# Performance work log

Measured on AMD Instinct MI355X. Metric: run time of the kernel, lower is better.

The kernel has to match this reference:

```python
import jax, jax.numpy as jnp
import numpy as np

N = 10000      # nodes
E = 160000     # edges
F_IN = 128     # input_feature
G = 64         # graphs in batch
NC = 10        # num_classes
H1, H2, H3 = 1000, 700, 200


def _xavier(k, fi, fo):
    lim = float(np.sqrt(6.0 / (fi + fo)))
    return jax.random.uniform(k, (fi, fo), jnp.float32, -lim, lim)


def setup_inputs() -> dict:
    key = jax.random.key(0)
    ks = jax.random.split(key, 8)
    x = jax.random.normal(ks[0], (N, F_IN), jnp.float32)
    edge_index = jax.random.randint(ks[1], (2, E), 0, N)
    batch = jnp.sort(jax.random.randint(ks[2], (N,), 0, G))
    return {
        "x": x,
        "edge_index": edge_index,
        "batch": batch,
        "W1": _xavier(ks[3], F_IN, H1), "b1": jnp.zeros((H1,), jnp.float32),
        "W2": _xavier(ks[4], H1, H2),   "b2": jnp.zeros((H2,), jnp.float32),
        "W3": _xavier(ks[5], H2, H3),   "b3": jnp.zeros((H3,), jnp.float32),
        "Wl": _xavier(ks[6], H3, NC),   "bl": jnp.zeros((NC,), jnp.float32),
    }


def _gcn_conv(x, W, b, src, dst, dinv):
    # GCNConv: h = xW; out_i = sum_{j->i} d_j^-1/2 d_i^-1/2 h_j + d_i^-1 h_i + b
    h = x @ W
    coef = dinv[src] * dinv[dst]                      # [E]
    agg = jax.ops.segment_sum(h[src] * coef[:, None], dst, num_segments=N)
    agg = agg + h * (dinv * dinv)[:, None]            # self-loop term
    return agg + b


def reference(x, edge_index, batch, W1, b1, W2, b2, W3, b3, Wl, bl):
    src, dst = edge_index[0], edge_index[1]
    # degree with self-loops (edge weight 1), computed on target nodes
    deg = jax.ops.segment_sum(jnp.ones((E,), x.dtype), dst, num_segments=N) + 1.0
    dinv = jax.lax.rsqrt(deg)

    h = jax.nn.relu(_gcn_conv(x, W1, b1, src, dst, dinv))
    h = jax.nn.relu(_gcn_conv(h, W2, b2, src, dst, dinv))
    h = jax.nn.relu(_gcn_conv(h, W3, b3, src, dst, dinv))

    # global_mean_pool over graph ids
    s = jax.ops.segment_sum(h, batch, num_segments=G)
    cnt = jax.ops.segment_sum(jnp.ones((N,), h.dtype), batch, num_segments=G)
    pooled = s / jnp.maximum(cnt, 1.0)[:, None]

    # dropout is identity in eval mode
    return pooled @ Wl + bl
```

## Files before the change

kernel.cpp:

```cpp
#include <hip/hip_runtime.h>
#include <hip/hip_bf16.h>
#include <stdint.h>


#define SLOT 64

__device__ __forceinline__ uint16_t f2b(float f) {
    union { float f; uint32_t u; } v; v.f = f;
    return (uint16_t)((v.u + 0x7fffu + ((v.u >> 16) & 1u)) >> 16);
}
__device__ __forceinline__ float blo(uint32_t u) { union { uint32_t u; float f; } v; v.u = u << 16; return v.f; }
__device__ __forceinline__ float bhi(uint32_t u) { union { uint32_t u; float f; } v; v.u = u & 0xffff0000u; return v.f; }

__global__ void k_scatter(const int* __restrict__ src, const int* __restrict__ dst,
                          int* __restrict__ cursor, int* __restrict__ slots, int E) {
    int e = blockIdx.x * blockDim.x + threadIdx.x;
    if (e < E) {
        int s = src[e], d = dst[e];
        int pos = atomicAdd(&cursor[d], 1);
        if (pos < SLOT) slots[d * SLOT + pos] = s;
    }
}

__global__ void k_prep(const float* __restrict__ W1, const float* __restrict__ W2,
                       const float* __restrict__ W3,
                       uint16_t* __restrict__ T1, uint16_t* __restrict__ T2,
                       uint16_t* __restrict__ T3,
                       const float* __restrict__ b1, const float* __restrict__ b2,
                       const float* __restrict__ b3,
                       float* __restrict__ p1, float* __restrict__ p2,
                       float* __restrict__ p3,
                       const float* __restrict__ x, uint16_t* __restrict__ xb,
                       const int* __restrict__ deg, float* __restrict__ dinv,
                       int N, int F, int H1, int H2, int H3,
                       int Fp, int H1p, int H2p, int H3p, int n8) {
    __shared__ float tile[32][33];
    int z = blockIdx.z;
    if (z < 3) {
        const float* W; uint16_t* T; int K, Nn, Kp, Np;
        if (z == 0)      { W = W1; T = T1; K = F;  Nn = H1; Kp = Fp;  Np = H1p; }
        else if (z == 1) { W = W2; T = T2; K = H1; Nn = H2; Kp = H1p; Np = H2p; }
        else             { W = W3; T = T3; K = H2; Nn = H3; Kp = H2p; Np = H3p; }
        if ((int)blockIdx.x * 32 >= Kp || (int)blockIdx.y * 32 >= Np) return;
        int k0 = blockIdx.x * 32, n0 = blockIdx.y * 32;
        int tx = threadIdx.x, ty = threadIdx.y;
        for (int i = ty; i < 32; i += 8) {
            int k = k0 + i, n = n0 + tx;
            tile[i][tx] = (k < K && n < Nn) ? W[(size_t)k * Nn + n] : 0.f;
        }
        __syncthreads();
        for (int i = ty; i < 32; i += 8) {
            int n = n0 + i, k = k0 + tx;
            T[(size_t)n * Kp + k] = f2b(tile[tx][i]);
        }
    } else {
        int id = (blockIdx.y * gridDim.x + blockIdx.x) * 256 + threadIdx.y * 32 + threadIdx.x;
        if (z == 3) {
            if (id < H1p) p1[id] = (id < H1) ? b1[id] : 0.f;
            else if (id < H1p + H2p) { int k = id - H1p; p2[k] = (k < H2) ? b2[k] : 0.f; }
            else if (id < H1p + H2p + H3p) { int k = id - H1p - H2p; p3[k] = (k < H3) ? b3[k] : 0.f; }
        } else if (z == 4) {
            if (id < n8) {
                int node = id / (F >> 3);
                float dv = rsqrtf((float)deg[node] + 1.0f);
                const float4* x4 = (const float4*)x;
                float4 a = x4[2 * id], b = x4[2 * id + 1];
                uint4 o;
                o.x = (uint32_t)f2b(a.x * dv) | ((uint32_t)f2b(a.y * dv) << 16);
                o.y = (uint32_t)f2b(a.z * dv) | ((uint32_t)f2b(a.w * dv) << 16);
                o.z = (uint32_t)f2b(b.x * dv) | ((uint32_t)f2b(b.y * dv) << 16);
                o.w = (uint32_t)f2b(b.z * dv) | ((uint32_t)f2b(b.w * dv) << 16);
                ((uint4*)xb)[id] = o;
            }
        } else {
            if (id < N) dinv[id] = rsqrtf((float)deg[id] + 1.0f);
        }
    }
}

__global__ __launch_bounds__(256) void k_agg_panel(
    const uint16_t* __restrict__ in, uint16_t* __restrict__ out,
    const int* __restrict__ deg_, const int* __restrict__ slots,
    const float* __restrict__ dinv, const float* __restrict__ bias,
    int N, int Hc, int pc, int P, int relu) {
    int slotg = blockIdx.x & 7;
    int panel = slotg % P;
    int seg   = slotg / P;
    int nseg  = 8 / P;
    int segLen = (N + nseg - 1) / nseg;
    int wave = threadIdx.x >> 6, lane = threadIdx.x & 63;
    int half = lane >> 5, sub = lane & 31;
    int item = (blockIdx.x >> 3) * 128 + wave * 32 + sub;
    int rel = item / pc;
    if (rel >= segLen) return;
    int node = seg * segLen + rel;
    if (node >= N) return;
    int j = panel * pc + (item - rel * pc);
    int deg = deg_[node];
    if (deg > SLOT) deg = SLOT;
    int base = node * SLOT;
    float dv = dinv[node];
    const uint4* in4 = (const uint4*)in;
    float a[8] = {0.f, 0.f, 0.f, 0.f, 0.f, 0.f, 0.f, 0.f};
    if (half == 0) {
        uint4 v = in4[(size_t)node * Hc + j];
        a[0] = blo(v.x); a[1] = bhi(v.x);
        a[2] = blo(v.y); a[3] = bhi(v.y);
        a[4] = blo(v.z); a[5] = bhi(v.z);
        a[6] = blo(v.w); a[7] = bhi(v.w);
    }
    int D8 = deg & ~7;
    int e = 4 * half;
    if (e < D8) {
        int4 q = *(const int4*)&slots[base + e];
        uint4 h0 = in4[(size_t)q.x * Hc + j];
        uint4 h1 = in4[(size_t)q.y * Hc + j];
        uint4 h2 = in4[(size_t)q.z * Hc + j];
        uint4 h3 = in4[(size_t)q.w * Hc + j];
        for (e += 8; e < D8; e += 8) {
            int4 qn = *(const int4*)&slots[base + e];
            uint4 g0 = in4[(size_t)qn.x * Hc + j];
            uint4 g1 = in4[(size_t)qn.y * Hc + j];
            uint4 g2 = in4[(size_t)qn.z * Hc + j];
            uint4 g3 = in4[(size_t)qn.w * Hc + j];
            a[0] += blo(h0.x); a[1] += bhi(h0.x);
            a[2] += blo(h0.y); a[3] += bhi(h0.y);
            a[4] += blo(h0.z); a[5] += bhi(h0.z);
            a[6] += blo(h0.w); a[7] += bhi(h0.w);
            a[0] += blo(h1.x); a[1] += bhi(h1.x);
            a[2] += blo(h1.y); a[3] += bhi(h1.y);
            a[4] += blo(h1.z); a[5] += bhi(h1.z);
            a[6] += blo(h1.w); a[7] += bhi(h1.w);
            a[0] += blo(h2.x); a[1] += bhi(h2.x);
            a[2] += blo(h2.y); a[3] += bhi(h2.y);
            a[4] += blo(h2.z); a[5] += bhi(h2.z);
            a[6] += blo(h2.w); a[7] += bhi(h2.w);
            a[0] += blo(h3.x); a[1] += bhi(h3.x);
            a[2] += blo(h3.y); a[3] += bhi(h3.y);
            a[4] += blo(h3.z); a[5] += bhi(h3.z);
            a[6] += blo(h3.w); a[7] += bhi(h3.w);
            h0 = g0; h1 = g1; h2 = g2; h3 = g3;
        }
        a[0] += blo(h0.x); a[1] += bhi(h0.x);
        a[2] += blo(h0.y); a[3] += bhi(h0.y);
        a[4] += blo(h0.z); a[5] += bhi(h0.z);
        a[6] += blo(h0.w); a[7] += bhi(h0.w);
        a[0] += blo(h1.x); a[1] += bhi(h1.x);
        a[2] += blo(h1.y); a[3] += bhi(h1.y);
        a[4] += blo(h1.z); a[5] += bhi(h1.z);
        a[6] += blo(h1.w); a[7] += bhi(h1.w);
        a[0] += blo(h2.x); a[1] += bhi(h2.x);
        a[2] += blo(h2.y); a[3] += bhi(h2.y);
        a[4] += blo(h2.z); a[5] += bhi(h2.z);
        a[6] += blo(h2.w); a[7] += bhi(h2.w);
        a[0] += blo(h3.x); a[1] += bhi(h3.x);
        a[2] += blo(h3.y); a[3] += bhi(h3.y);
        a[4] += blo(h3.z); a[5] += bhi(h3.z);
        a[6] += blo(h3.w); a[7] += bhi(h3.w);
    }
    int t0 = half ? (D8 + 4 < deg ? D8 + 4 : deg) : D8;
    int t1 = half ? deg : (D8 + 4 < deg ? D8 + 4 : deg);
    for (int ee = t0; ee < t1; ++ee) {
        int s0 = slots[base + ee];
        uint4 h = in4[(size_t)s0 * Hc + j];
        a[0] += blo(h.x); a[1] += bhi(h.x);
        a[2] += blo(h.y); a[3] += bhi(h.y);
        a[4] += blo(h.z); a[5] += bhi(h.z);
        a[6] += blo(h.w); a[7] += bhi(h.w);
    }
#pragma unroll
    for (int t = 0; t < 8; ++t) a[t] += __shfl_xor(a[t], 32, 64);
    if (half == 0) {
        if (bias) {
            const float4* b4 = (const float4*)bias;
            float4 b0 = b4[2 * j], b1 = b4[2 * j + 1];
            a[0] = fmaf(a[0], dv, b0.x); a[1] = fmaf(a[1], dv, b0.y);
            a[2] = fmaf(a[2], dv, b0.z); a[3] = fmaf(a[3], dv, b0.w);
            a[4] = fmaf(a[4], dv, b1.x); a[5] = fmaf(a[5], dv, b1.y);
            a[6] = fmaf(a[6], dv, b1.z); a[7] = fmaf(a[7], dv, b1.w);
        } else {
#pragma unroll
            for (int t = 0; t < 8; ++t) a[t] *= dv;
        }
        if (relu) {
#pragma unroll
            for (int t = 0; t < 8; ++t) a[t] = fmaxf(a[t], 0.f);
        }
        uint4 o;
        o.x = (uint32_t)f2b(a[0]) | ((uint32_t)f2b(a[1]) << 16);
        o.y = (uint32_t)f2b(a[2]) | ((uint32_t)f2b(a[3]) << 16);
        o.z = (uint32_t)f2b(a[4]) | ((uint32_t)f2b(a[5]) << 16);
        o.w = (uint32_t)f2b(a[6]) | ((uint32_t)f2b(a[7]) << 16);
        ((uint4*)out)[(size_t)node * Hc + j] = o;
    }
}

__global__ __launch_bounds__(256) void k_pool_fast(
    const uint16_t* __restrict__ h, const int* __restrict__ batch,
    float* __restrict__ pooled_sum, int N, int H, int Hp) {
    int j    = threadIdx.x & 63;
    int slot = threadIdx.x >> 6;
    int Hc   = H >> 2;
    if (j >= Hc) return;
    int HcP  = Hp >> 2;
    const uint2* h2 = (const uint2*)h;
    int base = (blockIdx.x * 4 + slot) * 16;
    float a0 = 0.f, a1 = 0.f, a2 = 0.f, a3 = 0.f;
    int gcur = -1;
#pragma unroll 4
    for (int t = 0; t < 16; ++t) {
        int node = base + t;
        if (node < N) {
            int g = batch[node];
            if (g != gcur) {
                if (gcur >= 0) {
                    float* ps = &pooled_sum[(size_t)gcur * H + j * 4];
                    atomicAdd(&ps[0], a0); atomicAdd(&ps[1], a1);
                    atomicAdd(&ps[2], a2); atomicAdd(&ps[3], a3);
                }
                gcur = g; a0 = a1 = a2 = a3 = 0.f;
            }
            uint2 v = h2[(size_t)node * HcP + j];
            a0 += blo(v.x); a1 += bhi(v.x);
            a2 += blo(v.y); a3 += bhi(v.y);
        }
    }
    if (gcur >= 0) {
        float* ps = &pooled_sum[(size_t)gcur * H + j * 4];
        atomicAdd(&ps[0], a0); atomicAdd(&ps[1], a1);
        atomicAdd(&ps[2], a2); atomicAdd(&ps[3], a3);
    }
}

typedef __attribute__((ext_vector_type(8))) short short8;
typedef __attribute__((ext_vector_type(4))) float floatx4;

#define LDSP(p) ((__attribute__((address_space(3))) void*)(uintptr_t)(p))
#define GLBP(p) ((const __attribute__((address_space(1))) void*)(uintptr_t)(p))

__global__ __launch_bounds__(256) void k_gemm128(
    const uint16_t* __restrict__ A, const uint16_t* __restrict__ Bt,
    const float* __restrict__ bias, uint16_t* __restrict__ Cout,
    int M, int Kp, int Np, int relu, int nrg, int nr,
    const float* __restrict__ rowscale) {
    int bid = blockIdx.x;
    int rsub = bid & 7;
    int t_ = bid >> 3;
    int rg = t_ % nrg, cc = t_ / nrg;
    int rt = rg * 8 + rsub;
    if (rt >= nr) return;
    int row0 = rt * 128, col0 = cc * 128;

    __shared__ uint16_t As[128 * 64];
    __shared__ uint16_t Bs[128 * 64];
    int tid = threadIdx.x;
    int wave = tid >> 6, lane = tid & 63;
    int quad = lane >> 4, m16 = lane & 15;
    int wr = wave >> 1, wc = wave & 1;

    int rA = tid >> 3;
    int cA = (tid & 7) ^ (rA & 7);
    const uint16_t* gA = A  + (size_t)(row0 + rA) * Kp + cA * 8;
    const uint16_t* gB = Bt + (size_t)(col0 + rA) * Kp + cA * 8;
    uint16_t* lA = As + tid * 8;
    uint16_t* lB = Bs + tid * 8;
    size_t rowStep32 = (size_t)32 * Kp;

    floatx4 acc[4][4];
#pragma unroll
    for (int i = 0; i < 4; ++i)
#pragma unroll
        for (int j = 0; j < 4; ++j) acc[i][j] = (floatx4){0.f, 0.f, 0.f, 0.f};

    const short* Ash = (const short*)As;
    const short* Bsh = (const short*)Bs;
    int swA = m16 & 7;

    for (int k0 = 0; k0 < Kp; k0 += 64) {
#pragma unroll
        for (int p = 0; p < 4; ++p) {
            __builtin_amdgcn_global_load_lds(GLBP(gA + p * rowStep32), LDSP(lA + p * 2048), 16, 0, 0);
            __builtin_amdgcn_global_load_lds(GLBP(gB + p * rowStep32), LDSP(lB + p * 2048), 16, 0, 0);
        }
        gA += 64; gB += 64;
        __syncthreads();
#pragma unroll
        for (int h = 0; h < 2; ++h) {
            short8 af[4], bf[4];
            int c = h * 4 + quad;
            int pos = (c ^ swA) * 8;
#pragma unroll
            for (int i = 0; i < 4; ++i)
                af[i] = *(const short8*)&Ash[(wr * 64 + i * 16 + m16) * 64 + pos];
#pragma unroll
            for (int j = 0; j < 4; ++j)
                bf[j] = *(const short8*)&Bsh[(wc * 64 + j * 16 + m16) * 64 + pos];
#pragma unroll
            for (int i = 0; i < 4; ++i)
#pragma unroll
                for (int j = 0; j < 4; ++j)
                    acc[i][j] = __builtin_amdgcn_mfma_f32_16x16x32_bf16(af[i], bf[j], acc[i][j], 0, 0, 0);
        }
        __syncthreads();
    }

    float bv[4];
#pragma unroll
    for (int j = 0; j < 4; ++j) {
        int n = col0 + wc * 64 + j * 16 + m16;
        bv[j] = bias ? bias[n] : 0.f;
    }
#pragma unroll
    for (int i = 0; i < 4; ++i) {
        int mBase = row0 + wr * 64 + i * 16 + quad * 4;
#pragma unroll
        for (int r = 0; r < 4; ++r) {
            int m = mBase + r;
            if (m < M) {
                float s = rowscale ? rowscale[m] : 1.f;
#pragma unroll
                for (int j = 0; j < 4; ++j) {
                    int n = col0 + wc * 64 + j * 16 + m16;
                    float v = acc[i][j][r] * s + bv[j];
                    if (relu) v = fmaxf(v, 0.f);
                    Cout[(size_t)m * Np + n] = f2b(v);
                }
            }
        }
    }
}

__global__ __launch_bounds__(256) void k_gemm64(
    const uint16_t* __restrict__ A, const uint16_t* __restrict__ Bt,
    const float* __restrict__ bias, uint16_t* __restrict__ Cout,
    int M, int Kp, int Np, int relu, int nrg, int nr,
    const float* __restrict__ rowscale) {
    int bid = blockIdx.x;
    int rsub = bid & 7;
    int t_ = bid >> 3;
    int rg = t_ % nrg, cc = t_ / nrg;
    int rt = rg * 8 + rsub;
    if (rt >= nr) return;
    int row0 = rt * 128, col0 = cc * 64;

    __shared__ uint16_t As[128 * 64];
    __shared__ uint16_t Bs[64 * 64];
    int tid = threadIdx.x;
    int wave = tid >> 6, lane = tid & 63;
    int quad = lane >> 4, m16 = lane & 15;
    int wr = wave >> 1, wc = wave & 1;

    int rA = tid >> 3;
    int cA = (tid & 7) ^ (rA & 7);
    const uint16_t* gA = A  + (size_t)(row0 + rA) * Kp + cA * 8;
    const uint16_t* gB = Bt + (size_t)(col0 + rA) * Kp + cA * 8;
    uint16_t* lA = As + tid * 8;
    uint16_t* lB = Bs + tid * 8;
    size_t rowStep32 = (size_t)32 * Kp;

    floatx4 acc[4][2];
#pragma unroll
    for (int i = 0; i < 4; ++i)
#pragma unroll
        for (int j = 0; j < 2; ++j) acc[i][j] = (floatx4){0.f, 0.f, 0.f, 0.f};

    const short* Ash = (const short*)As;
    const short* Bsh = (const short*)Bs;
    int swA = m16 & 7;

    for (int k0 = 0; k0 < Kp; k0 += 64) {
#pragma unroll
        for (int p = 0; p < 4; ++p)
            __builtin_amdgcn_global_load_lds(GLBP(gA + p * rowStep32), LDSP(lA + p * 2048), 16, 0, 0);
#pragma unroll
        for (int p = 0; p < 2; ++p)
            __builtin_amdgcn_global_load_lds(GLBP(gB + p * rowStep32), LDSP(lB + p * 2048), 16, 0, 0);
        gA += 64; gB += 64;
        __syncthreads();
#pragma unroll
        for (int h = 0; h < 2; ++h) {
            short8 af[4], bf[2];
            int c = h * 4 + quad;
            int pos = (c ^ swA) * 8;
#pragma unroll
            for (int i = 0; i < 4; ++i)
                af[i] = *(const short8*)&Ash[(wr * 64 + i * 16 + m16) * 64 + pos];
#pragma unroll
            for (int j = 0; j < 2; ++j)
                bf[j] = *(const short8*)&Bsh[(wc * 32 + j * 16 + m16) * 64 + pos];
#pragma unroll
            for (int i = 0; i < 4; ++i)
#pragma unroll
                for (int j = 0; j < 2; ++j)
                    acc[i][j] = __builtin_amdgcn_mfma_f32_16x16x32_bf16(af[i], bf[j], acc[i][j], 0, 0, 0);
        }
        __syncthreads();
    }

    float bv[2];
#pragma unroll
    for (int j = 0; j < 2; ++j) {
        int n = col0 + wc * 32 + j * 16 + m16;
        bv[j] = bias ? bias[n] : 0.f;
    }
#pragma unroll
    for (int i = 0; i < 4; ++i) {
        int mBase = row0 + wr * 64 + i * 16 + quad * 4;
#pragma unroll
        for (int r = 0; r < 4; ++r) {
            int m = mBase + r;
            if (m < M) {
                float s = rowscale ? rowscale[m] : 1.f;
#pragma unroll
                for (int j = 0; j < 2; ++j) {
                    int n = col0 + wc * 32 + j * 16 + m16;
                    float v = acc[i][j][r] * s + bv[j];
                    if (relu) v = fmaxf(v, 0.f);
                    Cout[(size_t)m * Np + n] = f2b(v);
                }
            }
        }
    }
}

__global__ void k_classifier(const float* __restrict__ pooled_sum,
                             const int* __restrict__ batch,
                             const float* __restrict__ Wl, const float* __restrict__ bl,
                             float* __restrict__ out, int N, int H, int NC) {
    int g = blockIdx.x, c = threadIdx.x;
    int lo = 0, hi = N;
    while (lo < hi) { int mid = (lo + hi) >> 1; if (batch[mid] < g) lo = mid + 1; else hi = mid; }
    int start = lo;
    lo = start; hi = N;
    while (lo < hi) { int mid = (lo + hi) >> 1; if (batch[mid] < g + 1) lo = mid + 1; else hi = mid; }
    int end = lo;
    float scale = 1.0f / fmaxf((float)(end - start), 1.0f);
    if (c < NC) {
        float acc = 0.f;
        for (int k = 0; k < H; ++k) acc += pooled_sum[(size_t)g * H + k] * Wl[(size_t)k * NC + c];
        out[(size_t)g * NC + c] = acc * scale + bl[c];
    }
}

static inline size_t align256(size_t x) { return (x + 255) & ~(size_t)255; }
static inline int pad128(int x) { return (x + 127) & ~127; }

extern "C" void kernel_launch(void* const* d_in, const int* in_sizes, int n_in,
                              void* d_out, int out_size, void* d_ws, size_t ws_size,
                              hipStream_t stream) {
    const float* x   = (const float*)d_in[0];
    const int*   ei  = (const int*)d_in[1];
    const int*   bat = (const int*)d_in[2];
    const float* W1  = (const float*)d_in[3];
    const float* b1  = (const float*)d_in[4];
    const float* W2  = (const float*)d_in[5];
    const float* b2  = (const float*)d_in[6];
    const float* W3  = (const float*)d_in[7];
    const float* b3  = (const float*)d_in[8];
    const float* Wl  = (const float*)d_in[9];
    const float* bl  = (const float*)d_in[10];

    const int N  = in_sizes[2];
    const int E  = in_sizes[1] / 2;
    const int F  = in_sizes[0] / N;
    const int H1 = in_sizes[4];
    const int H2 = in_sizes[6];
    const int H3 = in_sizes[8];
    const int NC = in_sizes[10];
    const int G  = out_size / NC;
    const int* src = ei;
    const int* dst = ei + E;

    const int Mp  = pad128(N);
    const int Fp  = F;
    const int H1p = pad128(H1);
    const int H2p = pad128(H2);
    const int H3p = pad128(H3);

    char* p = (char*)d_ws;
    size_t off = 0;
    auto carve = [&](size_t bytes) { void* q = p + off; off += align256(bytes); return q; };
    uint16_t* xb     = (uint16_t*)carve((size_t)Mp * Fp * 2);
    uint16_t* bufA   = (uint16_t*)carve((size_t)Mp * 2048);
    uint16_t* bufB   = (uint16_t*)carve((size_t)Mp * 2048);
    uint16_t* W1t    = (uint16_t*)carve((size_t)H1p * Fp * 2);
    uint16_t* W2t    = (uint16_t*)carve((size_t)H2p * H1p * 2);
    uint16_t* W3t    = (uint16_t*)carve((size_t)H3p * H2p * 2);
    float* b1p       = (float*)carve((size_t)H1p * 4);
    float* b2p       = (float*)carve((size_t)H2p * 4);
    float* b3p       = (float*)carve((size_t)H3p * 4);
    float* dinv      = (float*)carve((size_t)N * 4);
    int*   cursor    = (int*)carve((size_t)N * 4);
    float* pooled    = (float*)carve((size_t)G * H3 * 4);
    int*   slots     = (int*)carve((size_t)N * SLOT * 4);
    (void)ws_size;

    const int nbE = (E + 255) / 256;

    size_t zlen = (size_t)((char*)pooled - (char*)cursor) + (size_t)G * H3 * 4;
    hipMemsetAsync(cursor, 0, zlen, stream);

    k_scatter<<<nbE, 256, 0, stream>>>(src, dst, cursor, slots, E);

    k_prep<<<dim3(32, 32, 6), dim3(32, 8), 0, stream>>>(
        W1, W2, W3, W1t, W2t, W3t, b1, b2, b3, b1p, b2p, b3p, x, xb,
        cursor, dinv, N, F, H1, H2, H3, Fp, H1p, H2p, H3p, N * F / 8);

    auto agg_grid = [&](int P, int pc) {
        int nseg = 8 / P;
        int segLen = (N + nseg - 1) / nseg;
        return 8 * ((segLen * pc + 127) / 128);
    };

    const int nr  = Mp / 128;
    const int nrg = (nr + 7) / 8;

    k_agg_panel<<<agg_grid(1, 16), 256, 0, stream>>>(
        xb, bufA, cursor, slots, dinv, nullptr, N, 16, 16, 1, 0);
    k_gemm128<<<nrg * 8 * (H1p / 128), 256, 0, stream>>>(
        bufA, W1t, b1p, bufB, N, Fp, H1p, 1, nrg, nr, nullptr);

    k_gemm128<<<nrg * 8 * (H2p / 128), 256, 0, stream>>>(
        bufB, W2t, nullptr, bufA, N, H1p, H2p, 0, nrg, nr, dinv);
    k_agg_panel<<<agg_grid(8, 12), 256, 0, stream>>>(
        bufA, bufB, cursor, slots, dinv, b2p, N, 96, 12, 8, 1);

    k_gemm64<<<nrg * 8 * (H3p / 64), 256, 0, stream>>>(
        bufB, W3t, nullptr, bufA, N, H2p, H3p, 0, nrg, nr, dinv);
    k_agg_panel<<<agg_grid(4, 8), 256, 0, stream>>>(
        bufA, bufB, cursor, slots, dinv, b3p, N, 32, 8, 4, 1);

    k_pool_fast<<<(N + 63) / 64, 256, 0, stream>>>(
        (const uint16_t*)bufB, bat, pooled, N, H3, H3p);
    k_classifier<<<G, 64, 0, stream>>>(pooled, bat, Wl, bl, (float*)d_out, N, H3, NC);
}
```

Baseline: 234.8 us.

## Partition edge scatter by destination range, parallelize classifier, trim aggregation panel counts

```diff
diff --git a/kernel.cpp b/kernel.cpp
--- a/kernel.cpp
+++ b/kernel.cpp
@@ -12,13 +12,25 @@
 __device__ __forceinline__ float blo(uint32_t u) { union { uint32_t u; float f; } v; v.u = u << 16; return v.f; }
 __device__ __forceinline__ float bhi(uint32_t u) { union { uint32_t u; float f; } v; v.u = u & 0xffff0000u; return v.f; }
 
-__global__ void k_scatter(const int* __restrict__ src, const int* __restrict__ dst,
-                          int* __restrict__ cursor, int* __restrict__ slots, int E) {
-    int e = blockIdx.x * blockDim.x + threadIdx.x;
-    if (e < E) {
-        int s = src[e], d = dst[e];
-        int pos = atomicAdd(&cursor[d], 1);
-        if (pos < SLOT) slots[d * SLOT + pos] = s;
+__global__ __launch_bounds__(256) void k_scatter(
+    const int* __restrict__ src, const int* __restrict__ dst,
+    int* __restrict__ cursor, int* __restrict__ slots, int E, int N) {
+    int g  = blockIdx.x & 7;
+    int nb = gridDim.x >> 3;
+    int b  = blockIdx.x >> 3;
+    int seg = (N + 7) >> 3;
+    int lo = g * seg;
+    int hi = lo + seg; if (hi > N) hi = N;
+    int per = (E + nb - 1) / nb;
+    int e0 = b * per;
+    int e1 = e0 + per; if (e1 > E) e1 = E;
+    for (int e = e0 + threadIdx.x; e < e1; e += 256) {
+        int d = dst[e];
+        if (d >= lo && d < hi) {
+            int s = src[e];
+            int pos = atomicAdd(&cursor[d], 1);
+            if (pos < SLOT) slots[d * SLOT + pos] = s;
+        }
     }
 }
 
@@ -427,7 +439,9 @@
                              const int* __restrict__ batch,
                              const float* __restrict__ Wl, const float* __restrict__ bl,
                              float* __restrict__ out, int N, int H, int NC) {
-    int g = blockIdx.x, c = threadIdx.x;
+    int g = blockIdx.x;
+    int t = threadIdx.x;
+    int c = t & 15, q = t >> 4;
     int lo = 0, hi = N;
     while (lo < hi) { int mid = (lo + hi) >> 1; if (batch[mid] < g) lo = mid + 1; else hi = mid; }
     int start = lo;
@@ -435,11 +449,14 @@
     while (lo < hi) { int mid = (lo + hi) >> 1; if (batch[mid] < g + 1) lo = mid + 1; else hi = mid; }
     int end = lo;
     float scale = 1.0f / fmaxf((float)(end - start), 1.0f);
+    float acc = 0.f;
     if (c < NC) {
-        float acc = 0.f;
-        for (int k = 0; k < H; ++k) acc += pooled_sum[(size_t)g * H + k] * Wl[(size_t)k * NC + c];
-        out[(size_t)g * NC + c] = acc * scale + bl[c];
-    }
+        for (int k = q; k < H; k += 4)
+            acc += pooled_sum[(size_t)g * H + k] * Wl[(size_t)k * NC + c];
+    }
+    acc += __shfl_xor(acc, 16, 64);
+    acc += __shfl_xor(acc, 32, 64);
+    if (q == 0 && c < NC) out[(size_t)g * NC + c] = acc * scale + bl[c];
 }
 
 static inline size_t align256(size_t x) { return (x + 255) & ~(size_t)255; }
@@ -495,12 +512,10 @@
     int*   slots     = (int*)carve((size_t)N * SLOT * 4);
     (void)ws_size;
 
-    const int nbE = (E + 255) / 256;
-
     size_t zlen = (size_t)((char*)pooled - (char*)cursor) + (size_t)G * H3 * 4;
     hipMemsetAsync(cursor, 0, zlen, stream);
 
-    k_scatter<<<nbE, 256, 0, stream>>>(src, dst, cursor, slots, E);
+    k_scatter<<<8 * 160, 256, 0, stream>>>(src, dst, cursor, slots, E, N);
 
     k_prep<<<dim3(32, 32, 6), dim3(32, 8), 0, stream>>>(
         W1, W2, W3, W1t, W2t, W3t, b1, b2, b3, b1p, b2p, b3p, x, xb,
@@ -522,13 +537,13 @@
 
     k_gemm128<<<nrg * 8 * (H2p / 128), 256, 0, stream>>>(
         bufB, W2t, nullptr, bufA, N, H1p, H2p, 0, nrg, nr, dinv);
-    k_agg_panel<<<agg_grid(8, 12), 256, 0, stream>>>(
-        bufA, bufB, cursor, slots, dinv, b2p, N, 96, 12, 8, 1);
+    k_agg_panel<<<agg_grid(8, 11), 256, 0, stream>>>(
+        bufA, bufB, cursor, slots, dinv, b2p, N, 96, 11, 8, 1);
 
     k_gemm64<<<nrg * 8 * (H3p / 64), 256, 0, stream>>>(
         bufB, W3t, nullptr, bufA, N, H2p, H3p, 0, nrg, nr, dinv);
-    k_agg_panel<<<agg_grid(4, 8), 256, 0, stream>>>(
-        bufA, bufB, cursor, slots, dinv, b3p, N, 32, 8, 4, 1);
+    k_agg_panel<<<agg_grid(4, 7), 256, 0, stream>>>(
+        bufA, bufB, cursor, slots, dinv, b3p, N, 32, 7, 4, 1);
 
     k_pool_fast<<<(N + 63) / 64, 256, 0, stream>>>(
         (const uint16_t*)bufB, bat, pooled, N, H3, H3p);
```

Result: no change. 235.0 us (+0.1%).
